# Kernel optimization log

Measured on AMD Instinct MI355X. Metric: run time of the kernel, lower is better.

The kernel has to match this reference:

```python
import jax, jax.numpy as jnp
import numpy as np

N_HEADS = 16
ROPE_BASE = 10000.0


def apply_rope(x):
    # x: (b, h, t, d); rotate interleaved pairs along last dim, positions = t axis
    b, h, t, d = x.shape
    theta = 1.0 / (ROPE_BASE ** (jnp.arange(0, d, 2, dtype=jnp.float32) / d))  # (d/2,)
    ang = jnp.arange(t, dtype=jnp.float32)[:, None] * theta[None, :]           # (t, d/2)
    cos = jnp.cos(ang)[None, None]  # (1,1,t,d/2)
    sin = jnp.sin(ang)[None, None]
    xp = x.reshape(b, h, t, d // 2, 2)
    x0, x1 = xp[..., 0], xp[..., 1]
    o0 = x0 * cos - x1 * sin
    o1 = x1 * cos + x0 * sin
    return jnp.stack([o0, o1], axis=-1).reshape(b, h, t, d)


def setup_inputs() -> dict:
    key = jax.random.key(0)
    k1, k2, k3 = jax.random.split(key, 3)
    B, T, C = 2, 2048, 1024
    x = jax.random.normal(k1, (B, T, C), dtype=jnp.float32)
    w_qkv = jax.random.normal(k2, (3 * C, C), dtype=jnp.float32) * (1.0 / np.sqrt(C))
    w_proj = jax.random.normal(k3, (C, C), dtype=jnp.float32) * (1.0 / np.sqrt(C))
    return {"x": x, "w_qkv": w_qkv, "w_proj": w_proj}


def reference(x, w_qkv, w_proj):
    B, T, C = x.shape
    H = N_HEADS
    D = C // H
    # fused QKV projection: (b,t,3C)
    qkv = x @ w_qkv.T
    qkv = qkv.reshape(B, T, 3, H, D).transpose(2, 0, 3, 1, 4)  # (3, b, h, t, d)
    q, k, v = qkv[0], qkv[1], qkv[2]
    q = apply_rope(q)
    k = apply_rope(k)
    scale = 1.0 / jnp.sqrt(jnp.float32(D))
    scores = jnp.einsum('bhqd,bhkd->bhqk', q, k) * scale  # (b,h,t,t)
    causal = jnp.tril(jnp.ones((T, T), dtype=bool))
    scores = jnp.where(causal[None, None], scores, jnp.finfo(scores.dtype).min)
    attn = jax.nn.softmax(scores, axis=-1)
    y = jnp.einsum('bhqk,bhkd->bhqd', attn, v)  # (b,h,t,d)
    y = y.transpose(0, 2, 1, 3).reshape(B, T, C)
    return y @ w_proj.T
```

## Files before the change

kernel.cpp:

```cpp
#include <hip/hip_runtime.h>
#include <math.h>

#define B_ 2
#define T_ 2048
#define C_ 1024
#define H_ 16
#define D_ 64
#define NX_ 4194304
#define NWQ_ 3145728
#define NWP_ 1048576

typedef unsigned short u16;
typedef unsigned int u32;
typedef __bf16 bf16x8 __attribute__((ext_vector_type(8)));
typedef _Float16 f16x8 __attribute__((ext_vector_type(8)));
typedef __fp16 fp16x2 __attribute__((ext_vector_type(2)));
typedef float f32x4 __attribute__((ext_vector_type(4)));
typedef u16 u16x4 __attribute__((ext_vector_type(4)));

__device__ __forceinline__ u16 f2bf(float f) {
    union { float f; u32 u; } v; v.f = f;
    u32 r = v.u + 0x7fffu + ((v.u >> 16) & 1u);
    return (u16)(r >> 16);
}

#define GLD_LDS(g, l) \
    __builtin_amdgcn_global_load_lds( \
        (const __attribute__((address_space(1))) u32*)(const void*)(g), \
        (__attribute__((address_space(3))) u32*)(void*)(l), 16, 0, 0)

__global__ __launch_bounds__(256) void cast_all(const float* __restrict__ x,
                                                const float* __restrict__ wq,
                                                const float* __restrict__ wp,
                                                u16* __restrict__ out,
                                                float* __restrict__ tab) {
    const int bid = blockIdx.x;
    if (bid >= 8192) {
        const int k = (bid - 8192) * 256 + threadIdx.x;
        #pragma unroll
        for (int e = 0; e < 2; ++e) {
            const int pidx = 2 * k + e;
            const int t = pidx >> 5, i = pidx & 31;
            const float theta = __expf(-0.2878231366f * (float)i);
            float sn, cs;
            __sincosf((float)t * theta, &sn, &cs);
            *(float2*)(tab + pidx * 2) = make_float2(cs, sn);
        }
        return;
    }
    const int i = (bid * 256 + threadIdx.x) * 4;
    const float* src;
    int off;
    if (i < NX_) { src = x; off = i; }
    else if (i < NX_ + NWQ_) { src = wq; off = i - NX_; }
    else { src = wp; off = i - NX_ - NWQ_; }
    float4 v = *(const float4*)(src + off);
    u16x4 o;
    o.x = f2bf(v.x); o.y = f2bf(v.y); o.z = f2bf(v.z); o.w = f2bf(v.w);
    *(u16x4*)(out + i) = o;
}

template <int EPI, int DBUF, int BN>
__global__ __launch_bounds__(256) void gemm64(const u16* __restrict__ A,
                                              const u16* __restrict__ Bm,
                                              float* __restrict__ OutF,
                                              u16* __restrict__ qb,
                                              u16* __restrict__ kb,
                                              u16* __restrict__ vt,
                                              const float* __restrict__ tab,
                                              int M, int N, int K) {
    constexpr int NBUF = DBUF ? 2 : 1;
    constexpr int MI = (BN == 128) ? 4 : 2;
    constexpr int BCH = BN / 32;
    __shared__ u16 As[NBUF][128 * 64];
    __shared__ u16 Bs[NBUF][BN * 64];
    const int tid = threadIdx.x;
    const int lane = tid & 63;
    const int wave = tid >> 6;
    const int wm = (BN == 128) ? (wave >> 1) * 64 : wave * 32;
    const int wn = (BN == 128) ? (wave & 1) * 64 : 0;
    const int m0 = blockIdx.y * 128;
    const int n0 = blockIdx.x * BN;

    const int rl = lane >> 3;
    const int sg = ((lane & 7) ^ rl) * 8;
    const u16* gA[4]; const u16* gB[BCH];
    int lofA[4], lofB[BCH];
    #pragma unroll
    for (int c = 0; c < 4; ++c) {
        const int ca = wave * 4 + c;
        gA[c] = A + (size_t)(m0 + ca * 8 + rl) * K + sg;
        lofA[c] = ca * 512;
    }
    #pragma unroll
    for (int c = 0; c < BCH; ++c) {
        const int cb = wave * BCH + c;
        gB[c] = Bm + (size_t)(n0 + cb * 8 + rl) * K + sg;
        lofB[c] = cb * 512;
    }

    const int col = lane & 15;
    const int quad = lane >> 4;
    int aoff[2][MI], boff[2][4];
    #pragma unroll
    for (int ks = 0; ks < 2; ++ks) {
        #pragma unroll
        for (int i = 0; i < MI; ++i) {
            const int m = wm + i * 16 + col;
            aoff[ks][i] = (m >> 3) * 512 + (m & 7) * 64 +
                          ((((ks << 2) | quad)) ^ (m & 7)) * 8;
        }
        #pragma unroll
        for (int j = 0; j < 4; ++j) {
            const int n = wn + j * 16 + col;
            boff[ks][j] = (n >> 3) * 512 + (n & 7) * 64 +
                          ((((ks << 2) | quad)) ^ (n & 7)) * 8;
        }
    }

    f32x4 acc[MI][4] = {};

#define GEMM_STAGE(BUFI, KOFF)                                                 \
    {                                                                          \
        _Pragma("unroll")                                                      \
        for (int c = 0; c < 4; ++c)                                            \
            GLD_LDS(gA[c] + (KOFF), &As[BUFI][lofA[c]]);                       \
        _Pragma("unroll")                                                      \
        for (int c = 0; c < BCH; ++c)                                          \
            GLD_LDS(gB[c] + (KOFF), &Bs[BUFI][lofB[c]]);                       \
    }

#define GEMM_COMPUTE(ASB, BSB)                                                 \
    {                                                                          \
        _Pragma("unroll")                                                      \
        for (int ks = 0; ks < 2; ++ks) {                                       \
            bf16x8 a[MI], b[4];                                                \
            _Pragma("unroll")                                                  \
            for (int i = 0; i < MI; ++i)                                       \
                a[i] = *(const bf16x8*)((ASB) + aoff[ks][i]);                  \
            _Pragma("unroll")                                                  \
            for (int j = 0; j < 4; ++j)                                        \
                b[j] = *(const bf16x8*)((BSB) + boff[ks][j]);                  \
            _Pragma("unroll")                                                  \
            for (int i = 0; i < MI; ++i)                                       \
                _Pragma("unroll")                                              \
                for (int j = 0; j < 4; ++j)                                    \
                    acc[i][j] = __builtin_amdgcn_mfma_f32_16x16x32_bf16(       \
                        a[i], b[j], acc[i][j], 0, 0, 0);                       \
        }                                                                      \
    }

    if (DBUF) {
        GEMM_STAGE(0, 0)
        __syncthreads();
        int buf = 0;
        for (int k0 = 64; k0 < K; k0 += 64) {
            GEMM_STAGE(buf ^ 1, k0)
            GEMM_COMPUTE(&As[buf][0], &Bs[buf][0])
            __syncthreads();
            buf ^= 1;
        }
        GEMM_COMPUTE(&As[buf][0], &Bs[buf][0])
    } else {
        for (int k0 = 0; k0 < K; k0 += 64) {
            __syncthreads();
            GEMM_STAGE(0, k0)
            __syncthreads();
            GEMM_COMPUTE(&As[0][0], &Bs[0][0])
        }
    }
#undef GEMM_COMPUTE
#undef GEMM_STAGE

    const int rq = quad * 4;
    if (EPI == 0) {
        #pragma unroll
        for (int i = 0; i < MI; ++i)
            #pragma unroll
            for (int j = 0; j < 4; ++j)
                #pragma unroll
                for (int r = 0; r < 4; ++r)
                    OutF[(size_t)(m0 + wm + i * 16 + rq + r) * N +
                         n0 + wn + j * 16 + col] = acc[i][j][r];
    } else {
        const int sslot = m0 >> 10;
        #pragma unroll
        for (int i = 0; i < MI; ++i) {
            const int gm = m0 + wm + i * 16 + rq;
            const int hh = (gm >> 6) & 15;
            const int dbase = gm & 63;
            #pragma unroll
            for (int j = 0; j < 4; ++j) {
                const int gt = n0 + wn + j * 16 + col;
                const int bb = gt >> 11;
                const int t = gt & (T_ - 1);
                const int bh = bb * H_ + hh;
                if (sslot < 2) {
                    const float4 cs4 = *(const float4*)(tab + t * 64 + dbase);
                    u16x4 ov;
                    ov[0] = f2bf(acc[i][j][0] * cs4.x - acc[i][j][1] * cs4.y);
                    ov[1] = f2bf(acc[i][j][1] * cs4.x + acc[i][j][0] * cs4.y);
                    ov[2] = f2bf(acc[i][j][2] * cs4.z - acc[i][j][3] * cs4.w);
                    ov[3] = f2bf(acc[i][j][3] * cs4.z + acc[i][j][2] * cs4.w);
                    u16* dst = (sslot == 0 ? qb : kb) +
                               ((size_t)bh * T_ + t) * D_ + dbase;
                    *(u16x4*)dst = ov;
                } else {
                    #pragma unroll
                    for (int r = 0; r < 4; ++r) {
                        union { _Float16 h; u16 u; } cv;
                        cv.h = (_Float16)acc[i][j][r];
                        vt[((size_t)bh * D_ + dbase + r) * T_ + t] = cv.u;
                    }
                }
            }
        }
    }
}

__global__ __launch_bounds__(256) void attn_mfma(const u16* __restrict__ qb,
                                                 const u16* __restrict__ kb,
                                                 const u16* __restrict__ vtg,
                                                 u16* __restrict__ y) {
    __shared__ u16 Ks[2][2 * 4096];
    __shared__ u16 Vt[2][2 * 4096];
    const int id = blockIdx.x;
    const int bh = id & 31;
    const int pr = id >> 5;
    const int b = bh >> 4, h = bh & 15;
    const int tid = threadIdx.x;
    const int lane = tid & 63;
    const int wave = tid >> 6;
    const int col = lane & 15;
    const int quad = lane >> 4;

    const int rl = lane >> 3;
    const int sg = ((lane & 7) ^ rl) * 8;
    const u16* kg[2]; const u16* vg[2];
    int lco[2];
    #pragma unroll
    for (int e = 0; e < 2; ++e) {
        const int ca = 2 * wave + e;
        kg[e] = kb + ((size_t)bh * T_ + ca * 8 + rl) * D_ + sg;
        vg[e] = vtg + ((size_t)bh * D_ + ca * 8 + rl) * T_ + sg;
        lco[e] = ca * 512;
    }

    int koff[2][4];
    #pragma unroll
    for (int ks = 0; ks < 2; ++ks)
        #pragma unroll
        for (int n = 0; n < 4; ++n) {
            const int rr = n * 16 + col;
            koff[ks][n] = (rr >> 3) * 512 + (rr & 7) * 64 +
                          ((((ks << 2) | quad)) ^ (rr & 7)) * 8;
        }

    const int srcA = col + ((quad & 1) << 5);
    const int srcB = srcA + 16;
    const bool hi = (quad >> 1) != 0;

#define STAGE2(BUF, C0)                                                        \
    {                                                                          \
        const size_t jj = (size_t)(C0) * 64;                                   \
        _Pragma("unroll")                                                      \
        for (int e = 0; e < 2; ++e) {                                          \
            GLD_LDS(kg[e] + jj * D_, &Ks[BUF][lco[e]]);                        \
            GLD_LDS(vg[e] + jj, &Vt[BUF][lco[e]]);                             \
            GLD_LDS(kg[e] + (jj + 64) * D_, &Ks[BUF][4096 + lco[e]]);          \
            GLD_LDS(vg[e] + jj + 64, &Vt[BUF][4096 + lco[e]]);                 \
        }                                                                      \
    }

#define CHUNK_COMPUTE(BUF, SUB, J0, DIAG)                                      \
    {                                                                          \
        const int j0_ = (J0);                                                  \
        const u16* ksb = &Ks[BUF][(SUB) * 4096];                               \
        const u16* vsb = &Vt[BUF][(SUB) * 4096];                               \
                                 \
        f32x4 s[4] = {};                                                       \
        __builtin_amdgcn_s_setprio(1);                                         \
        _Pragma("unroll")                                                      \
        for (int ks = 0; ks < 2; ++ks)                                         \
            _Pragma("unroll")                                                  \
            for (int n = 0; n < 4; ++n) {                                      \
                const bf16x8 kf = *(const bf16x8*)(ksb + koff[ks][n]);         \
                s[n] = __builtin_amdgcn_mfma_f32_16x16x32_bf16(                \
                    kf, qf[ks], s[n], 0, 0, 0);                                \
            }                                                                  \
        __builtin_amdgcn_s_setprio(0);                                         \
              \
        u32 pk[4][2];                                                          \
        _Pragma("unroll")                                                      \
        for (int n = 0; n < 4; ++n) {                                          \
            float p[4];                                                        \
            _Pragma("unroll")                                                  \
            for (int r = 0; r < 4; ++r) {                                      \
                float pv = __builtin_amdgcn_exp2f(s[n][r] * 0.1803368801f);    \
                if (DIAG && (j0_ + n * 16 + quad * 4 + r > qrow)) pv = 0.0f;   \
                p[r] = pv;                                                     \
                lsv[r] += pv;                                                  \
            }                                                                  \
            union { fp16x2 h; u32 u; } c0, c1;                                 \
            c0.h = __builtin_amdgcn_cvt_pkrtz(p[0], p[1]);                     \
            c1.h = __builtin_amdgcn_cvt_pkrtz(p[2], p[3]);                     \
            pk[n][0] = c0.u;                                                   \
            pk[n][1] = c1.u;                                                   \
        }                                                                      \
                         \
        _Pragma("unroll")                                                      \
        for (int ks = 0; ks < 2; ++ks) {                                       \
            const int nl = 2 * ks, nh = nl + 1;                                \
            const u32 w0a = __shfl(pk[nl][0], srcA);                           \
            const u32 w0b = __shfl(pk[nh][0], srcA);                           \
            const u32 w1a = __shfl(pk[nl][1], srcA);                           \
            const u32 w1b = __shfl(pk[nh][1], srcA);                           \
            const u32 w2a = __shfl(pk[nl][0], srcB);                           \
            const u32 w2b = __shfl(pk[nh][0], srcB);                           \
            const u32 w3a = __shfl(pk[nl][1], srcB);                           \
            const u32 w3b = __shfl(pk[nh][1], srcB);                           \
            union { u32 u[4]; f16x8 v; } af;                                   \
            af.u[0] = hi ? w0b : w0a;                                          \
            af.u[1] = hi ? w1b : w1a;                                          \
            af.u[2] = hi ? w2b : w2a;                                          \
            af.u[3] = hi ? w3b : w3a;                                          \
            __builtin_amdgcn_s_setprio(1);                                     \
            _Pragma("unroll")                                                  \
            for (int n = 0; n < 4; ++n) {                                      \
                const f16x8 vf = *(const f16x8*)(vsb + koff[ks][n]);           \
                o[n] = __builtin_amdgcn_mfma_f32_16x16x32_f16(                 \
                    af.v, vf, o[n], 0, 0, 0);                                  \
            }                                                                  \
            __builtin_amdgcn_s_setprio(0);                                     \
        }                                                                      \
    }

    for (int half = 0; half < 2; ++half) {
        const int qt = half ? pr : (31 - pr);
        const int q0 = qt * 64;
        const int qrow = q0 + wave * 16 + col;
        const int nchunks = qt + 1;
        const int niter = (nchunks + 1) >> 1;

        const u16* qbase = qb + ((size_t)bh * T_ + q0 + wave * 16) * D_;
        bf16x8 qf[2];
        #pragma unroll
        for (int ks = 0; ks < 2; ++ks)
            qf[ks] = *(const bf16x8*)(qbase + col * D_ + ks * 32 + quad * 8);

        f32x4 o[4] = {};
        float lsv[4] = {};

        __syncthreads();
        STAGE2(0, 0)

        int buf = 0;
        for (int it = 0; it + 1 < niter; ++it) {
            __syncthreads();
            STAGE2(buf ^ 1, 2 * (it + 1))
            CHUNK_COMPUTE(buf, 0, it * 128, false)
            CHUNK_COMPUTE(buf, 1, it * 128 + 64, false)
            buf ^= 1;
        }
        __syncthreads();
        if (nchunks & 1) {
            CHUNK_COMPUTE(buf, 0, (nchunks - 1) * 64, true)
        } else {
            CHUNK_COMPUTE(buf, 0, (nchunks - 2) * 64, false)
            CHUNK_COMPUTE(buf, 1, (nchunks - 1) * 64, true)
        }

        float l = (lsv[0] + lsv[1]) + (lsv[2] + lsv[3]);
        l += __shfl_xor(l, 16);
        l += __shfl_xor(l, 32);
        const float inv = 1.0f / l;
        float invr[4];
        #pragma unroll
        for (int r = 0; r < 4; ++r)
            invr[r] = __shfl(inv, quad * 4 + r);
        #pragma unroll
        for (int r = 0; r < 4; ++r) {
            const int row = q0 + wave * 16 + quad * 4 + r;
            u16* yp = y + (size_t)(b * T_ + row) * C_ + h * D_;
            #pragma unroll
            for (int n = 0; n < 4; ++n)
                yp[n * 16 + col] = f2bf(o[n][r] * invr[r]);
        }
    }
#undef CHUNK_COMPUTE
#undef STAGE2
}

extern "C" void kernel_launch(void* const* d_in, const int* in_sizes, int n_in,
                              void* d_out, int out_size, void* d_ws, size_t ws_size,
                              hipStream_t stream) {
    const float* x      = (const float*)d_in[0];
    const float* w_qkv  = (const float*)d_in[1];
    const float* w_proj = (const float*)d_in[2];
    float* out = (float*)d_out;

    const int M = B_ * T_;
    u16* xb  = (u16*)d_ws;
    u16* wqb = xb + NX_;
    u16* wpb = wqb + NWQ_;
    u16* qb  = wpb + NWP_;
    u16* kb  = qb + NX_;
    u16* vt  = kb + NX_;
    u16* yb  = vt + NX_;
    float* tab = (float*)(yb + NX_);

    cast_all<<<8192 + 128, 256, 0, stream>>>(x, w_qkv, w_proj, xb, tab);

    gemm64<1, 1, 64><<<dim3(M / 64, 3 * C_ / 128), 256, 0, stream>>>(
        wqb, xb, nullptr, qb, kb, vt, tab, 3 * C_, M, C_);

    attn_mfma<<<512, 256, 0, stream>>>(qb, kb, vt, yb);

    gemm64<0, 1, 64><<<dim3(C_ / 64, M / 128), 256, 0, stream>>>(
        yb, wpb, out, nullptr, nullptr, nullptr, nullptr, M, C_, C_);
}
```

Baseline: 174.5 us.

## Process both paired query tiles in one K/V sweep to share staged tiles

Each block previously handled its high and low causal query tiles one after the other, streaming K/V from global into LDS once per tile. Now both tiles' Q fragments and accumulators stay live together, and a single pass over the high tile's K/V chunks also updates the low tile for chunks up to its diagonal. This removes the second K/V load sweep and its barriers. In exchange it roughly doubles accumulator register pressure, which may lower occupancy, and adds branches inside the loop.

```diff
diff --git a/kernel.cpp b/kernel.cpp
--- a/kernel.cpp
+++ b/kernel.cpp
@@ -260,6 +260,27 @@
     const int srcB = srcA + 16;
     const bool hi = (quad >> 1) != 0;
 
+    const int qt_h = 31 - pr, qt_l = pr;
+    const int q0h = qt_h * 64, q0l = qt_l * 64;
+    const int qrh = q0h + wave * 16 + col;
+    const int qrl = q0l + wave * 16 + col;
+    const int nch = qt_h + 1;
+    const int niter = (nch + 1) >> 1;
+
+    bf16x8 qfh[2], qfl[2];
+    {
+        const u16* qbh = qb + ((size_t)bh * T_ + q0h + wave * 16) * D_;
+        const u16* qbl = qb + ((size_t)bh * T_ + q0l + wave * 16) * D_;
+        #pragma unroll
+        for (int ks = 0; ks < 2; ++ks) {
+            qfh[ks] = *(const bf16x8*)(qbh + col * D_ + ks * 32 + quad * 8);
+            qfl[ks] = *(const bf16x8*)(qbl + col * D_ + ks * 32 + quad * 8);
+        }
+    }
+
+    f32x4 oh[4] = {}, ol[4] = {};
+    float lsh[4] = {}, lsl[4] = {};
+
 #define STAGE2(BUF, C0)                                                        \
     {                                                                          \
         const size_t jj = (size_t)(C0) * 64;                                   \
@@ -272,12 +293,11 @@
         }                                                                      \
     }
 
-#define CHUNK_COMPUTE(BUF, SUB, J0, DIAG)                                      \
+#define CC(BUF, SUB, J0, DIAG, QF, O, LSV, QROW)                               \
     {                                                                          \
         const int j0_ = (J0);                                                  \
         const u16* ksb = &Ks[BUF][(SUB) * 4096];                               \
         const u16* vsb = &Vt[BUF][(SUB) * 4096];                               \
-                                 \
         f32x4 s[4] = {};                                                       \
         __builtin_amdgcn_s_setprio(1);                                         \
         _Pragma("unroll")                                                      \
@@ -286,10 +306,9 @@
             for (int n = 0; n < 4; ++n) {                                      \
                 const bf16x8 kf = *(const bf16x8*)(ksb + koff[ks][n]);         \
                 s[n] = __builtin_amdgcn_mfma_f32_16x16x32_bf16(                \
-                    kf, qf[ks], s[n], 0, 0, 0);                                \
+                    kf, (QF)[ks], s[n], 0, 0, 0);                              \
             }                                                                  \
         __builtin_amdgcn_s_setprio(0);                                         \
-              \
         u32 pk[4][2];                                                          \
         _Pragma("unroll")                                                      \
         for (int n = 0; n < 4; ++n) {                                          \
@@ -297,17 +316,17 @@
             _Pragma("unroll")                                                  \
             for (int r = 0; r < 4; ++r) {                                      \
                 float pv = __builtin_amdgcn_exp2f(s[n][r] * 0.1803368801f);    \
-                if (DIAG && (j0_ + n * 16 + quad * 4 + r > qrow)) pv = 0.0f;   \
+                if ((DIAG) && (j0_ + n * 16 + quad * 4 + r > (QROW)))          \
+                    pv = 0.0f;                                                 \
                 p[r] = pv;                                                     \
-                lsv[r] += pv;                                                  \
+                (LSV)[r] += pv;                                                \
             }                                                                  \
-            union { fp16x2 h; u32 u; } c0, c1;                                 \
-            c0.h = __builtin_amdgcn_cvt_pkrtz(p[0], p[1]);                     \
-            c1.h = __builtin_amdgcn_cvt_pkrtz(p[2], p[3]);                     \
-            pk[n][0] = c0.u;                                                   \
-            pk[n][1] = c1.u;                                                   \
+            union { fp16x2 h; u32 u; } c0u, c1u;                               \
+            c0u.h = __builtin_amdgcn_cvt_pkrtz(p[0], p[1]);                    \
+            c1u.h = __builtin_amdgcn_cvt_pkrtz(p[2], p[3]);                    \
+            pk[n][0] = c0u.u;                                                  \
+            pk[n][1] = c1u.u;                                                  \
         }                                                                      \
-                         \
         _Pragma("unroll")                                                      \
         for (int ks = 0; ks < 2; ++ks) {                                       \
             const int nl = 2 * ks, nh = nl + 1;                                \
@@ -328,67 +347,59 @@
             _Pragma("unroll")                                                  \
             for (int n = 0; n < 4; ++n) {                                      \
                 const f16x8 vf = *(const f16x8*)(vsb + koff[ks][n]);           \
-                o[n] = __builtin_amdgcn_mfma_f32_16x16x32_f16(                 \
-                    af.v, vf, o[n], 0, 0, 0);                                  \
+                (O)[n] = __builtin_amdgcn_mfma_f32_16x16x32_f16(               \
+                    af.v, vf, (O)[n], 0, 0, 0);                                \
             }                                                                  \
             __builtin_amdgcn_s_setprio(0);                                     \
         }                                                                      \
     }
 
-    for (int half = 0; half < 2; ++half) {
-        const int qt = half ? pr : (31 - pr);
-        const int q0 = qt * 64;
-        const int qrow = q0 + wave * 16 + col;
-        const int nchunks = qt + 1;
-        const int niter = (nchunks + 1) >> 1;
-
-        const u16* qbase = qb + ((size_t)bh * T_ + q0 + wave * 16) * D_;
-        bf16x8 qf[2];
-        #pragma unroll
-        for (int ks = 0; ks < 2; ++ks)
-            qf[ks] = *(const bf16x8*)(qbase + col * D_ + ks * 32 + quad * 8);
-
-        f32x4 o[4] = {};
-        float lsv[4] = {};
-
+    STAGE2(0, 0)
+
+    int buf = 0;
+    for (int it = 0; it + 1 < niter; ++it) {
         __syncthreads();
-        STAGE2(0, 0)
-
-        int buf = 0;
-        for (int it = 0; it + 1 < niter; ++it) {
-            __syncthreads();
-            STAGE2(buf ^ 1, 2 * (it + 1))
-            CHUNK_COMPUTE(buf, 0, it * 128, false)
-            CHUNK_COMPUTE(buf, 1, it * 128 + 64, false)
-            buf ^= 1;
-        }
-        __syncthreads();
-        if (nchunks & 1) {
-            CHUNK_COMPUTE(buf, 0, (nchunks - 1) * 64, true)
-        } else {
-            CHUNK_COMPUTE(buf, 0, (nchunks - 2) * 64, false)
-            CHUNK_COMPUTE(buf, 1, (nchunks - 1) * 64, true)
-        }
-
-        float l = (lsv[0] + lsv[1]) + (lsv[2] + lsv[3]);
-        l += __shfl_xor(l, 16);
-        l += __shfl_xor(l, 32);
-        const float inv = 1.0f / l;
-        float invr[4];
-        #pragma unroll
-        for (int r = 0; r < 4; ++r)
-            invr[r] = __shfl(inv, quad * 4 + r);
-        #pragma unroll
-        for (int r = 0; r < 4; ++r) {
-            const int row = q0 + wave * 16 + quad * 4 + r;
-            u16* yp = y + (size_t)(b * T_ + row) * C_ + h * D_;
-            #pragma unroll
-            for (int n = 0; n < 4; ++n)
-                yp[n * 16 + col] = f2bf(o[n][r] * invr[r]);
-        }
-    }
-#undef CHUNK_COMPUTE
+        STAGE2(buf ^ 1, 2 * (it + 1))
+        const int c0 = 2 * it, c1 = c0 + 1;
+        CC(buf, 0, c0 * 64, false, qfh, oh, lsh, qrh)
+        if (c0 <= qt_l) CC(buf, 0, c0 * 64, c0 == qt_l, qfl, ol, lsl, qrl)
+        CC(buf, 1, c1 * 64, false, qfh, oh, lsh, qrh)
+        if (c1 <= qt_l) CC(buf, 1, c1 * 64, c1 == qt_l, qfl, ol, lsl, qrl)
+        buf ^= 1;
+    }
+    __syncthreads();
+    if (nch & 1) {
+        CC(buf, 0, (nch - 1) * 64, true, qfh, oh, lsh, qrh)
+    } else {
+        CC(buf, 0, (nch - 2) * 64, false, qfh, oh, lsh, qrh)
+        CC(buf, 1, (nch - 1) * 64, true, qfh, oh, lsh, qrh)
+    }
+
+#undef CC
 #undef STAGE2
+
+#define EPI_WRITE(O, LSV, Q0)                                                  \
+    {                                                                          \
+        float l = ((LSV)[0] + (LSV)[1]) + ((LSV)[2] + (LSV)[3]);               \
+        l += __shfl_xor(l, 16);                                                \
+        l += __shfl_xor(l, 32);                                                \
+        const float inv = 1.0f / l;                                            \
+        float invr[4];                                                         \
+        _Pragma("unroll")                                                      \
+        for (int r = 0; r < 4; ++r)                                            \
+            invr[r] = __shfl(inv, quad * 4 + r);                               \
+        _Pragma("unroll")                                                      \
+        for (int r = 0; r < 4; ++r) {                                          \
+            const int row = (Q0) + wave * 16 + quad * 4 + r;                   \
+            u16* yp = y + (size_t)(b * T_ + row) * C_ + h * D_;                \
+            _Pragma("unroll")                                                  \
+            for (int n = 0; n < 4; ++n)                                        \
+                yp[n * 16 + col] = f2bf((O)[n][r] * invr[r]);                  \
+        }                                                                      \
+    }
+    EPI_WRITE(oh, lsh, q0h)
+    EPI_WRITE(ol, lsl, q0l)
+#undef EPI_WRITE
 }
 
 extern "C" void kernel_launch(void* const* d_in, const int* in_sizes, int n_in,
```

New measurement: 173.3 us. About the same (-0.7%).
